# Performance work log

Hardware: AMD Instinct MI355X
Metric: run time of the kernel (lower is better)

The kernel has to match this reference:

```python
import jax, jax.numpy as jnp
import numpy as np

IMG_W, IMG_H = 640, 480
OS = 8            # roialign output_size
SCALE = 1.0       # spatial_scale (boxes already mapped to feature coords)
ALIGNED = True
ALPHA = 1.0       # student-t alpha


def _roi_align_one(feat, boxes):
    # feat: [C, H, W]; boxes: [sn, 4] (x1, y1, x2, y2) in feature coords.
    # torchvision RoIAlign, sampling_ratio=1 (one sample at each bin center).
    C, H, W = feat.shape
    off = 0.5 if ALIGNED else 0.0
    x1 = boxes[:, 0] * SCALE - off
    y1 = boxes[:, 1] * SCALE - off
    x2 = boxes[:, 2] * SCALE - off
    y2 = boxes[:, 3] * SCALE - off
    bw = (x2 - x1) / OS   # bin width  [sn]
    bh = (y2 - y1) / OS   # bin height [sn]
    grid = jnp.arange(OS, dtype=feat.dtype) + 0.5
    xs = x1[:, None] + grid * bw[:, None]   # [sn, OS]
    ys = y1[:, None] + grid * bh[:, None]   # [sn, OS]
    X = jnp.broadcast_to(xs[:, None, :], (xs.shape[0], OS, OS))  # [sn,OS,OS]
    Y = jnp.broadcast_to(ys[:, :, None], (ys.shape[0], OS, OS))
    valid = (Y >= -1.0) & (Y <= H) & (X >= -1.0) & (X <= W)
    y = jnp.clip(Y, 0.0, H - 1)
    x = jnp.clip(X, 0.0, W - 1)
    y0f = jnp.floor(y); x0f = jnp.floor(x)
    y0 = y0f.astype(jnp.int32); x0 = x0f.astype(jnp.int32)
    y1i = jnp.minimum(y0 + 1, H - 1); x1i = jnp.minimum(x0 + 1, W - 1)
    ly = y - y0f; lx = x - x0f
    hy = 1.0 - ly; hx = 1.0 - lx
    def g(yi, xi):
        return feat[:, yi, xi]  # [C, sn, OS, OS]
    val = (hy * hx)[None] * g(y0, x0) + (hy * lx)[None] * g(y0, x1i) \
        + (ly * hx)[None] * g(y1i, x0) + (ly * lx)[None] * g(y1i, x1i)
    val = jnp.where(valid[None], val, 0.0)
    return jnp.transpose(val, (1, 0, 2, 3))  # [sn, C, OS, OS]


def setup_inputs() -> dict:
    key = jax.random.key(0)
    ks = jax.random.split(key, 10)
    B, SN, C, T, FY, FX = 16, 64, 480, 2, 60, 80
    NDF1, NDF2, K = 1024, 256, 64
    z = jax.random.normal(ks[0], (B, C, T, FY, FX), jnp.float32)
    # boxes in image pixel coords
    cx = jax.random.uniform(ks[1], (B, SN), minval=0.1, maxval=0.9) * IMG_W
    cy = jax.random.uniform(ks[2], (B, SN), minval=0.1, maxval=0.9) * IMG_H
    bw = jax.random.uniform(ks[3], (B, SN), minval=0.05, maxval=0.3) * IMG_W
    bh = jax.random.uniform(ks[4], (B, SN), minval=0.05, maxval=0.3) * IMG_H
    x1 = jnp.clip(cx - bw / 2, 0.0, IMG_W); x2 = jnp.clip(cx + bw / 2, 0.0, IMG_W)
    y1 = jnp.clip(cy - bh / 2, 0.0, IMG_H); y2 = jnp.clip(cy + bh / 2, 0.0, IMG_H)
    bboxs = jnp.stack([x1, y1, x2, y2], axis=-1).astype(jnp.float32)
    din = C * OS * OS
    w1 = jax.random.normal(ks[5], (NDF1, din), jnp.float32) * (din ** -0.5)
    b1 = jnp.zeros((NDF1,), jnp.float32)
    w2 = jax.random.normal(ks[6], (NDF2, NDF1), jnp.float32) * (NDF1 ** -0.5)
    b2 = jnp.zeros((NDF2,), jnp.float32)
    centroids = jax.random.normal(ks[7], (K, NDF2), jnp.float32)
    return {"z": z, "bboxs": bboxs, "w1": w1, "b1": b1, "w2": w2, "b2": b2,
            "centroids": centroids}


def reference(z, bboxs, w1, b1, w2, b2, centroids):
    B, C, T, fy, fx = z.shape
    sn = bboxs.shape[1]
    # scale image-space boxes to feature coords (per (x,y) pair as in torch code)
    sc = jnp.array([fx / IMG_W, fy / IMG_H], jnp.float32)
    bb = (bboxs.reshape(B, sn, 2, 2) * sc).reshape(B, sn, 4)
    bb = jnp.nan_to_num(bb)
    feat = z[:, :, -1]  # [B, C, fy, fx]
    pooled = jax.vmap(_roi_align_one)(feat, bb)  # [B, sn, C, OS, OS]
    flat = pooled.reshape(B * sn, -1)
    e = flat @ w1.T + b1
    e = e @ w2.T + b2
    zz = e.reshape(B, sn, -1)  # [B, sn, ndf2]
    # student-t soft assignment (faithful: L2 norm, not squared)
    z2 = jnp.sum(zz * zz, axis=-1, keepdims=True)          # [B,sn,1]
    c2 = jnp.sum(centroids * centroids, axis=-1)           # [K]
    zc = jnp.einsum('bsd,kd->bsk', zz, centroids)          # [B,sn,K]
    nrm = jnp.sqrt(jnp.maximum(z2 + c2 - 2.0 * zc, 0.0))
    s = ((1.0 + nrm) / ALPHA) ** (-(ALPHA + 1.0) / 2.0)
    s = s / jnp.sum(s, axis=-1, keepdims=True)
    c = jnp.argmax(s, axis=2)
    return zz, s, c
```

## Files before the change

kernel.cpp:

```cpp
#include <hip/hip_runtime.h>
#include <hip/hip_bf16.h>

static constexpr int B_  = 16;
static constexpr int SN_ = 64;
static constexpr int C_  = 480;
static constexpr int T_  = 2;
static constexpr int FY_ = 60;
static constexpr int FX_ = 80;
static constexpr int OS_ = 8;
static constexpr int DIN = 30720;
static constexpr int M_  = 1024;
static constexpr int N1_ = 1024;
static constexpr int N2_ = 256;
static constexpr int K_  = 64;
static constexpr int SPLITK = 32;
static constexpr int CH_ZZ  = 3 * DIN / SPLITK;
static constexpr int NIT_ZZ = CH_ZZ / 64;
static constexpr int NIT_FW = 3 * N1_ / 64;
static constexpr int CPB = 2;
static constexpr int IMG = FY_ * FX_;
static constexpr int NB_ROI = 16 * (C_ / CPB);
static constexpr int NB_W1T = (DIN / 64) * (N1_ / 64);
static constexpr int NB_W2P = N2_;

typedef __bf16 bf16x8 __attribute__((ext_vector_type(8)));
typedef float  f32x4  __attribute__((ext_vector_type(4)));
typedef unsigned int u32_as1 __attribute__((address_space(1)));
typedef unsigned int u32_as3 __attribute__((address_space(3)));

__device__ __forceinline__ float bf2f(unsigned short u) {
    union { unsigned int i; float f; } v; v.i = ((unsigned int)u) << 16; return v.f;
}
__device__ __forceinline__ unsigned short f2bf(float f) {
    unsigned int u = __float_as_uint(f);
    u = u + 0x7FFFu + ((u >> 16) & 1u);
    return (unsigned short)(u >> 16);
}
__device__ __forceinline__ void gll16(const void* g, void* l) {
    __builtin_amdgcn_global_load_lds((const u32_as1*)g, (u32_as3*)l, 16, 0, 0);
}

template<int NIT, int SEG>
__device__ __forceinline__ void gemm_core(
    const unsigned short* __restrict__ Abase, long long Astride,
    const unsigned short* __restrict__ Bbase, long long Bstride,
    int kv0, f32x4 (&acc)[4][4],
    unsigned short* As, unsigned short* Bs)
{
    const int t = threadIdx.x;
    const int w = t >> 6, lane = t & 63;
    const int rl8 = lane >> 3, slot = lane & 7;
    const int wm = w >> 1, wn = w & 1;
    const int fr = lane & 15, fg = lane >> 4;
    const int swz8 = (slot ^ rl8) * 8;

    long long arow[4], brow[4];
    int ci[4];
#pragma unroll
    for (int c = 0; c < 4; ++c) {
        ci[c] = w * 4 + c;
        const int row = ci[c] * 8 + rl8;
        arow[c] = (long long)row * Astride;
        brow[c] = (long long)row * Bstride;
    }

    auto stage = [&](int it, int par) {
        const int kv  = kv0 + it * 64;
        const int seg = (kv >= 2 * SEG) ? 2 : ((kv >= SEG) ? 1 : 0);
        const int kin = kv - seg * SEG;
        const int aoff = kin + ((seg == 2) ? SEG : 0) + swz8;
        const int boff = kin + ((seg == 1) ? SEG : 0) + swz8;
#pragma unroll
        for (int c = 0; c < 4; ++c) {
            gll16(Abase + arow[c] + aoff, (char*)As + par * 16384 + ci[c] * 1024);
            gll16(Bbase + brow[c] + boff, (char*)Bs + par * 16384 + ci[c] * 1024);
        }
    };

    stage(0, 0);
    stage(1, 1);

    for (int it = 0; it < NIT; ++it) {
        const int par = it & 1;
        if (it + 1 < NIT) asm volatile("s_waitcnt vmcnt(8)" ::: "memory");
        else              asm volatile("s_waitcnt vmcnt(0)" ::: "memory");
        __builtin_amdgcn_s_barrier();

        const char* Ab = (const char*)As + par * 16384;
        const char* Bb = (const char*)Bs + par * 16384;
        bf16x8 a[2][4], b[2][4];
#pragma unroll
        for (int ks = 0; ks < 2; ++ks)
#pragma unroll
            for (int mf = 0; mf < 4; ++mf) {
                const int row = wm * 64 + mf * 16 + fr;
                a[ks][mf] = *reinterpret_cast<const bf16x8*>(
                    Ab + row * 128 + 16 * ((ks * 4 + fg) ^ (fr & 7)));
            }
#pragma unroll
        for (int ks = 0; ks < 2; ++ks)
#pragma unroll
            for (int nf = 0; nf < 4; ++nf) {
                const int row = wn * 64 + nf * 16 + fr;
                b[ks][nf] = *reinterpret_cast<const bf16x8*>(
                    Bb + row * 128 + 16 * ((ks * 4 + fg) ^ (fr & 7)));
            }
        asm volatile("s_waitcnt lgkmcnt(0)" ::: "memory");
        __builtin_amdgcn_sched_barrier(0);
        __builtin_amdgcn_s_barrier();
        __builtin_amdgcn_sched_barrier(0);
        if (it + 2 < NIT) stage(it + 2, par);

        __builtin_amdgcn_s_setprio(1);
#pragma unroll
        for (int ks = 0; ks < 2; ++ks)
#pragma unroll
            for (int mf = 0; mf < 4; ++mf)
#pragma unroll
                for (int nf = 0; nf < 4; ++nf)
                    acc[mf][nf] = __builtin_amdgcn_mfma_f32_16x16x32_bf16(
                        a[ks][mf], b[ks][nf], acc[ks ? mf : mf][nf], 0, 0, 0);
        __builtin_amdgcn_s_setprio(0);
    }
}

__global__ __launch_bounds__(256) void prep_kernel(
    const float* __restrict__ z, const float* __restrict__ bboxs,
    const float* __restrict__ w1, const float* __restrict__ w2,
    const float* __restrict__ b1, const float* __restrict__ b2,
    unsigned short* __restrict__ flat2, unsigned short* __restrict__ w1T2,
    unsigned short* __restrict__ w2cat, float* __restrict__ bf) {
    __shared__ __align__(16) char smem[39424];
    const int blk = blockIdx.x;
    const int t = threadIdx.x;

    if (blk < NB_ROI) {
        float* img = (float*)smem;
        float (*bxc)[4] = (float (*)[4])(smem + 38400);
        const int b  = blk / (C_ / CPB);
        const int cg = blk % (C_ / CPB);
        const float* zb = z + ((size_t)b * C_ + (size_t)cg * CPB) * (size_t)(T_ * IMG)
                            + (size_t)(T_ - 1) * IMG;
#pragma unroll
        for (int c = 0; c < CPB; ++c) {
            const float4* src = (const float4*)(zb + (size_t)c * (T_ * IMG));
            float4* dst = (float4*)(img + c * IMG);
            for (int i = t; i < IMG / 4; i += 256) dst[i] = src[i];
        }
        if (t < 64) {
            const float* bp = bboxs + ((size_t)b * 64 + t) * 4;
            const float v0 = bp[0], v1 = bp[1], v2 = bp[2], v3 = bp[3];
            bxc[t][0] = isnan(v0) ? 0.f : v0;
            bxc[t][1] = isnan(v1) ? 0.f : v1;
            bxc[t][2] = isnan(v2) ? 0.f : v2;
            bxc[t][3] = isnan(v3) ? 0.f : v3;
        }
        __syncthreads();

        const int p = t & 63, mh = t >> 6;
        const int gy = p >> 3, gx = p & 7;
        for (int mq = 0; mq < 16; ++mq) {
            const int m = mq * 4 + mh;
            const float x1 = bxc[m][0] * 0.125f - 0.5f;
            const float y1 = bxc[m][1] * 0.125f - 0.5f;
            const float x2 = bxc[m][2] * 0.125f - 0.5f;
            const float y2 = bxc[m][3] * 0.125f - 0.5f;
            const float bw = (x2 - x1) * (1.0f / OS_);
            const float bh = (y2 - y1) * (1.0f / OS_);
            const float X = x1 + ((float)gx + 0.5f) * bw;
            const float Y = y1 + ((float)gy + 0.5f) * bh;
            const bool valid = (Y >= -1.0f) && (Y <= (float)FY_) &&
                               (X >= -1.0f) && (X <= (float)FX_);
            const float yc = fminf(fmaxf(Y, 0.f), (float)(FY_ - 1));
            const float xc = fminf(fmaxf(X, 0.f), (float)(FX_ - 1));
            const float y0f = floorf(yc), x0f = floorf(xc);
            const int y0 = (int)y0f, x0 = (int)x0f;
            const int y1i = min(y0 + 1, FY_ - 1);
            const int x1i = min(x0 + 1, FX_ - 1);
            const float ly = yc - y0f, lx = xc - x0f;
            const float hy = 1.f - ly,  hx = 1.f - lx;
            float w00 = hy * hx, w01 = hy * lx, w10 = ly * hx, w11 = ly * lx;
            if (!valid) { w00 = 0.f; w01 = 0.f; w10 = 0.f; w11 = 0.f; }
            const int i00 = y0 * FX_ + x0, i01 = y0 * FX_ + x1i;
            const int i10 = y1i * FX_ + x0, i11 = y1i * FX_ + x1i;
            unsigned short* fo = flat2 + (size_t)(b * 64 + m) * (2 * DIN)
                                       + cg * (CPB * 64) + p;
#pragma unroll
            for (int c = 0; c < CPB; ++c) {
                const float* f = img + c * IMG;
                const float v = w00 * f[i00] + w01 * f[i01] + w10 * f[i10] + w11 * f[i11];
                const unsigned short hi = f2bf(v);
                const unsigned short lo = f2bf(v - bf2f(hi));
                fo[c * 64]       = hi;
                fo[DIN + c * 64] = lo;
            }
        }
    } else if (blk < NB_ROI + NB_W1T) {
        float (*L)[65] = (float (*)[65])smem;
        const int idx = blk - NB_ROI;
        const int q0 = (idx % (DIN / 64)) * 64, j0 = (idx / (DIN / 64)) * 64;
        const int tr = t >> 4, tc4 = (t & 15) * 4;
#pragma unroll
        for (int jj = 0; jj < 4; ++jj) {
            const int j = jj * 16 + tr;
            const float4 v = *(const float4*)(w1 + (size_t)(j0 + j) * DIN + q0 + tc4);
            L[j][tc4] = v.x; L[j][tc4 + 1] = v.y; L[j][tc4 + 2] = v.z; L[j][tc4 + 3] = v.w;
        }
        __syncthreads();
#pragma unroll
        for (int pass = 0; pass < 4; ++pass) {
            const int ql = pass * 16 + tr;
            const int jc = tc4;
            ushort4 h4, l4;
            float v0 = L[jc + 0][ql], v1 = L[jc + 1][ql], v2 = L[jc + 2][ql], v3 = L[jc + 3][ql];
            h4.x = f2bf(v0); l4.x = f2bf(v0 - bf2f(h4.x));
            h4.y = f2bf(v1); l4.y = f2bf(v1 - bf2f(h4.y));
            h4.z = f2bf(v2); l4.z = f2bf(v2 - bf2f(h4.z));
            h4.w = f2bf(v3); l4.w = f2bf(v3 - bf2f(h4.w));
            *(ushort4*)(w1T2 + (size_t)(q0 + ql) * 2048 + j0 + jc)        = h4;
            *(ushort4*)(w1T2 + (size_t)(q0 + ql) * 2048 + 1024 + j0 + jc) = l4;
        }
    } else {
        float* red = (float*)smem;
        const int p = blk - (NB_ROI + NB_W1T);
        float acc = 0.f;
#pragma unroll
        for (int j = t; j < N1_; j += 256) {
            const float v = w2[(size_t)p * N1_ + j];
            const unsigned short hi = f2bf(v);
            const unsigned short lo = f2bf(v - bf2f(hi));
            w2cat[(size_t)p * 2048 + j]        = hi;
            w2cat[(size_t)p * 2048 + 1024 + j] = lo;
            acc = fmaf(v, b1[j], acc);
        }
        red[t] = acc; __syncthreads();
        for (int s = 128; s > 0; s >>= 1) { if (t < s) red[t] += red[t + s]; __syncthreads(); }
        if (t == 0) bf[p] = red[0] + b2[p];
    }
}

__global__ __launch_bounds__(256, 2) void fusew_mfma(const unsigned short* __restrict__ w2cat,
                                                     const unsigned short* __restrict__ w1T2,
                                                     unsigned short* __restrict__ W2) {
    __shared__ __align__(16) unsigned short As[2 * 128 * 64];
    __shared__ __align__(16) unsigned short Bs[2 * 128 * 64];
    const int pb = blockIdx.x, qb = blockIdx.y;
    f32x4 acc[4][4];
#pragma unroll
    for (int i = 0; i < 4; ++i)
#pragma unroll
        for (int j = 0; j < 4; ++j) acc[i][j] = (f32x4){0.f, 0.f, 0.f, 0.f};

    gemm_core<NIT_FW, N1_>(w2cat + (long long)pb * 128 * 2048, 2048,
                           w1T2 + (long long)qb * 128 * 2048, 2048,
                           0, acc, As, Bs);

    const int t = threadIdx.x;
    const int w = t >> 6, lane = t & 63;
    const int wm = w >> 1, wn = w & 1;
    const int fr = lane & 15, fg = lane >> 4;
#pragma unroll
    for (int mf = 0; mf < 4; ++mf)
#pragma unroll
        for (int nf = 0; nf < 4; ++nf)
#pragma unroll
            for (int r = 0; r < 4; ++r) {
                const int p = pb * 128 + wm * 64 + mf * 16 + fg * 4 + r;
                const int q = qb * 128 + wn * 64 + nf * 16 + fr;
                const float v = acc[mf][nf][r];
                const unsigned short hi = f2bf(v);
                const unsigned short lo = f2bf(v - bf2f(hi));
                W2[(size_t)p * (2 * DIN) + q]       = hi;
                W2[(size_t)p * (2 * DIN) + DIN + q] = lo;
            }
}

__global__ __launch_bounds__(256, 2) void zz_mfma(const unsigned short* __restrict__ flat2,
                                                  const unsigned short* __restrict__ W2,
                                                  float* __restrict__ part) {
    __shared__ __align__(16) unsigned short As[2 * 128 * 64];
    __shared__ __align__(16) unsigned short Bs[2 * 128 * 64];
    const int nb = blockIdx.x, mb = blockIdx.y, sp = blockIdx.z;
    f32x4 acc[4][4];
#pragma unroll
    for (int i = 0; i < 4; ++i)
#pragma unroll
        for (int j = 0; j < 4; ++j) acc[i][j] = (f32x4){0.f, 0.f, 0.f, 0.f};

    gemm_core<NIT_ZZ, DIN>(flat2 + (long long)mb * 128 * (2 * DIN), 2 * DIN,
                           W2 + (long long)nb * 128 * (2 * DIN), 2 * DIN,
                           sp * CH_ZZ, acc, As, Bs);

    float* po = part + (size_t)sp * (M_ * N2_);
    const int t = threadIdx.x;
    const int w = t >> 6, lane = t & 63;
    const int wm = w >> 1, wn = w & 1;
    const int fr = lane & 15, fg = lane >> 4;
#pragma unroll
    for (int mf = 0; mf < 4; ++mf)
#pragma unroll
        for (int nf = 0; nf < 4; ++nf)
#pragma unroll
            for (int r = 0; r < 4; ++r) {
                const int m = mb * 128 + wm * 64 + mf * 16 + fg * 4 + r;
                const int n = nb * 128 + wn * 64 + nf * 16 + fr;
                po[(size_t)m * N2_ + n] = acc[mf][nf][r];
            }
}

__global__ __launch_bounds__(256) void reduce_cluster_kernel(
    const float* __restrict__ part, const float* __restrict__ bf,
    const float* __restrict__ cent,
    float* __restrict__ out_zz, float* __restrict__ out_s, float* __restrict__ out_c) {
    __shared__ float row[N2_];
    const int m = blockIdx.x, t = threadIdx.x;
    float a = bf[t];
#pragma unroll
    for (int s = 0; s < SPLITK; ++s) a += part[(size_t)s * (M_ * N2_) + (size_t)m * N2_ + t];
    out_zz[(size_t)m * N2_ + t] = a;
    row[t] = a;
    __syncthreads();
    if (t < 64) {
        const float* cr = cent + (size_t)t * N2_;
        float dot = 0.f, c2 = 0.f, z2 = 0.f;
        for (int d = 0; d < N2_; ++d) {
            const float zv = row[d], cv = cr[d];
            dot = fmaf(zv, cv, dot);
            c2  = fmaf(cv, cv, c2);
            z2  = fmaf(zv, zv, z2);
        }
        const float nrm = sqrtf(fmaxf(z2 + c2 - 2.f * dot, 0.f));
        const float su = 1.0f / (1.0f + nrm);
        float ssum = su;
#pragma unroll
        for (int mk = 1; mk < 64; mk <<= 1) ssum += __shfl_xor(ssum, mk, 64);
        const float s = su / ssum;
        out_s[(size_t)m * 64 + t] = s;
        float bv = s; int bi = t;
#pragma unroll
        for (int mk = 1; mk < 64; mk <<= 1) {
            const float ov = __shfl_xor(bv, mk, 64);
            const int   oi = __shfl_xor(bi, mk, 64);
            if (ov > bv || (ov == bv && oi < bi)) { bv = ov; bi = oi; }
        }
        if (t == 0) out_c[m] = (float)bi;
    }
}

extern "C" void kernel_launch(void* const* d_in, const int* in_sizes, int n_in,
                              void* d_out, int out_size, void* d_ws, size_t ws_size,
                              hipStream_t stream) {
    const float* z     = (const float*)d_in[0];
    const float* bboxs = (const float*)d_in[1];
    const float* w1    = (const float*)d_in[2];
    const float* b1    = (const float*)d_in[3];
    const float* w2    = (const float*)d_in[4];
    const float* b2    = (const float*)d_in[5];
    const float* cent  = (const float*)d_in[6];
    float* out = (float*)d_out;
    float* out_zz = out;
    float* out_s  = out + (size_t)M_ * N2_;
    float* out_c  = out + (size_t)M_ * N2_ + (size_t)M_ * K_;

    char* ws = (char*)d_ws;
    unsigned short* w1T2   = (unsigned short*)(ws);
    unsigned short* flat2  = (unsigned short*)(ws + 125829120u);
    unsigned short* W2     = (unsigned short*)(ws + 251658240u);
    float*          part   = (float*)(ws + 283115520u);
    unsigned short* w2cat  = (unsigned short*)(ws + 316669952u);
    float*          bfused = (float*)(ws + 317718528u);

    prep_kernel<<<dim3(NB_ROI + NB_W1T + NB_W2P), dim3(256), 0, stream>>>(
        z, bboxs, w1, w2, b1, b2, flat2, w1T2, w2cat, bfused);
    fusew_mfma<<<dim3(2, 240), dim3(256), 0, stream>>>(w2cat, w1T2, W2);
    zz_mfma<<<dim3(2, 8, SPLITK), dim3(256), 0, stream>>>(flat2, W2, part);
    reduce_cluster_kernel<<<dim3(1024), dim3(256), 0, stream>>>(part, bfused, cent,
                                                                out_zz, out_s, out_c);
}
```

Before: 273.8 us.

## Restructure split-bf16 GEMMs to stage hi/lo halves together with 8-wave blocks

The shared GEMM core now loads the hi and lo halves of A and B for the same k-chunk into LDS together, instead of walking three concatenated k-segments. Each step issues the three hi*hi, hi*lo and lo*hi MFMAs, so the A/B fragments are reused across the three products. Blocks grow to 512 threads arranged as 2x4 waves with a 64 KB-per-stage LDS double buffer. Block indices are remapped to a 1D grid so that tiles sharing an operand land on the same XCD. The aim is better operand reuse and L2 locality, at the cost of occupancy, which drops to one block per CU with larger LDS use.

```diff
diff --git a/kernel.cpp b/kernel.cpp
--- a/kernel.cpp
+++ b/kernel.cpp
@@ -14,9 +14,8 @@
 static constexpr int N2_ = 256;
 static constexpr int K_  = 64;
 static constexpr int SPLITK = 32;
-static constexpr int CH_ZZ  = 3 * DIN / SPLITK;
-static constexpr int NIT_ZZ = CH_ZZ / 64;
-static constexpr int NIT_FW = 3 * N1_ / 64;
+static constexpr int NCH_ZZ = (DIN / 64) / SPLITK;
+static constexpr int NCH_FW = N1_ / 64;
 static constexpr int CPB = 2;
 static constexpr int IMG = FY_ * FX_;
 static constexpr int NB_ROI = 16 * (C_ / CPB);
@@ -40,76 +39,78 @@
     __builtin_amdgcn_global_load_lds((const u32_as1*)g, (u32_as3*)l, 16, 0, 0);
 }
 
-template<int NIT, int SEG>
+template<int NCHUNK, int SEG>
 __device__ __forceinline__ void gemm_core(
     const unsigned short* __restrict__ Abase, long long Astride,
     const unsigned short* __restrict__ Bbase, long long Bstride,
-    int kv0, f32x4 (&acc)[4][4],
-    unsigned short* As, unsigned short* Bs)
+    int k0, f32x4 (&acc)[4][2], unsigned short* L)
 {
     const int t = threadIdx.x;
     const int w = t >> 6, lane = t & 63;
     const int rl8 = lane >> 3, slot = lane & 7;
-    const int wm = w >> 1, wn = w & 1;
+    const int wm = w >> 2, wn = w & 3;
     const int fr = lane & 15, fg = lane >> 4;
     const int swz8 = (slot ^ rl8) * 8;
 
-    long long arow[4], brow[4];
-    int ci[4];
-#pragma unroll
-    for (int c = 0; c < 4; ++c) {
-        ci[c] = w * 4 + c;
+    long long arow[2], brow[2];
+    int ci[2];
+#pragma unroll
+    for (int c = 0; c < 2; ++c) {
+        ci[c] = w * 2 + c;
         const int row = ci[c] * 8 + rl8;
         arow[c] = (long long)row * Astride;
         brow[c] = (long long)row * Bstride;
     }
 
-    auto stage = [&](int it, int par) {
-        const int kv  = kv0 + it * 64;
-        const int seg = (kv >= 2 * SEG) ? 2 : ((kv >= SEG) ? 1 : 0);
-        const int kin = kv - seg * SEG;
-        const int aoff = kin + ((seg == 2) ? SEG : 0) + swz8;
-        const int boff = kin + ((seg == 1) ? SEG : 0) + swz8;
-#pragma unroll
-        for (int c = 0; c < 4; ++c) {
-            gll16(Abase + arow[c] + aoff, (char*)As + par * 16384 + ci[c] * 1024);
-            gll16(Bbase + brow[c] + boff, (char*)Bs + par * 16384 + ci[c] * 1024);
+    auto stage = [&](int chunk, int par) {
+        const int kin = k0 + chunk * 64;
+        char* Lp = (char*)L + par * 65536;
+#pragma unroll
+        for (int c = 0; c < 2; ++c) {
+            gll16(Abase + arow[c] + kin + swz8,       Lp + 0 * 16384 + ci[c] * 1024);
+            gll16(Abase + arow[c] + SEG + kin + swz8, Lp + 1 * 16384 + ci[c] * 1024);
+            gll16(Bbase + brow[c] + kin + swz8,       Lp + 2 * 16384 + ci[c] * 1024);
+            gll16(Bbase + brow[c] + SEG + kin + swz8, Lp + 3 * 16384 + ci[c] * 1024);
         }
     };
 
     stage(0, 0);
     stage(1, 1);
 
-    for (int it = 0; it < NIT; ++it) {
+    for (int it = 0; it < NCHUNK; ++it) {
         const int par = it & 1;
-        if (it + 1 < NIT) asm volatile("s_waitcnt vmcnt(8)" ::: "memory");
-        else              asm volatile("s_waitcnt vmcnt(0)" ::: "memory");
+        if (it + 1 < NCHUNK) asm volatile("s_waitcnt vmcnt(8)" ::: "memory");
+        else                 asm volatile("s_waitcnt vmcnt(0)" ::: "memory");
         __builtin_amdgcn_s_barrier();
 
-        const char* Ab = (const char*)As + par * 16384;
-        const char* Bb = (const char*)Bs + par * 16384;
-        bf16x8 a[2][4], b[2][4];
-#pragma unroll
-        for (int ks = 0; ks < 2; ++ks)
-#pragma unroll
-            for (int mf = 0; mf < 4; ++mf) {
-                const int row = wm * 64 + mf * 16 + fr;
-                a[ks][mf] = *reinterpret_cast<const bf16x8*>(
-                    Ab + row * 128 + 16 * ((ks * 4 + fg) ^ (fr & 7)));
-            }
-#pragma unroll
-        for (int ks = 0; ks < 2; ++ks)
-#pragma unroll
-            for (int nf = 0; nf < 4; ++nf) {
-                const int row = wn * 64 + nf * 16 + fr;
-                b[ks][nf] = *reinterpret_cast<const bf16x8*>(
-                    Bb + row * 128 + 16 * ((ks * 4 + fg) ^ (fr & 7)));
-            }
+        const char* Lp = (const char*)L + par * 65536;
+        bf16x8 a[2][2][4], b[2][2][2];
+#pragma unroll
+        for (int hl = 0; hl < 2; ++hl)
+#pragma unroll
+            for (int ks = 0; ks < 2; ++ks)
+#pragma unroll
+                for (int mf = 0; mf < 4; ++mf) {
+                    const int row = wm * 64 + mf * 16 + fr;
+                    a[hl][ks][mf] = *reinterpret_cast<const bf16x8*>(
+                        Lp + hl * 16384 + row * 128 + 16 * ((ks * 4 + fg) ^ (fr & 7)));
+                }
+#pragma unroll
+        for (int hl = 0; hl < 2; ++hl)
+#pragma unroll
+            for (int ks = 0; ks < 2; ++ks)
+#pragma unroll
+                for (int nf = 0; nf < 2; ++nf) {
+                    const int row = wn * 32 + nf * 16 + fr;
+                    b[hl][ks][nf] = *reinterpret_cast<const bf16x8*>(
+                        Lp + (2 + hl) * 16384 + row * 128 + 16 * ((ks * 4 + fg) ^ (fr & 7)));
+                }
         asm volatile("s_waitcnt lgkmcnt(0)" ::: "memory");
         __builtin_amdgcn_sched_barrier(0);
         __builtin_amdgcn_s_barrier();
         __builtin_amdgcn_sched_barrier(0);
-        if (it + 2 < NIT) stage(it + 2, par);
+        if (it + 2 < NCHUNK) stage(it + 2, par);
+        __builtin_amdgcn_sched_barrier(0);
 
         __builtin_amdgcn_s_setprio(1);
 #pragma unroll
@@ -117,9 +118,14 @@
 #pragma unroll
             for (int mf = 0; mf < 4; ++mf)
 #pragma unroll
-                for (int nf = 0; nf < 4; ++nf)
+                for (int nf = 0; nf < 2; ++nf) {
                     acc[mf][nf] = __builtin_amdgcn_mfma_f32_16x16x32_bf16(
-                        a[ks][mf], b[ks][nf], acc[ks ? mf : mf][nf], 0, 0, 0);
+                        a[0][ks][mf], b[0][ks][nf], acc[mf][nf], 0, 0, 0);
+                    acc[mf][nf] = __builtin_amdgcn_mfma_f32_16x16x32_bf16(
+                        a[0][ks][mf], b[1][ks][nf], acc[mf][nf], 0, 0, 0);
+                    acc[mf][nf] = __builtin_amdgcn_mfma_f32_16x16x32_bf16(
+                        a[1][ks][mf], b[0][ks][nf], acc[mf][nf], 0, 0, 0);
+                }
         __builtin_amdgcn_s_setprio(0);
     }
 }
@@ -239,34 +245,36 @@
     }
 }
 
-__global__ __launch_bounds__(256, 2) void fusew_mfma(const unsigned short* __restrict__ w2cat,
+__global__ __launch_bounds__(512, 1) void fusew_mfma(const unsigned short* __restrict__ w2cat,
                                                      const unsigned short* __restrict__ w1T2,
                                                      unsigned short* __restrict__ W2) {
-    __shared__ __align__(16) unsigned short As[2 * 128 * 64];
-    __shared__ __align__(16) unsigned short Bs[2 * 128 * 64];
-    const int pb = blockIdx.x, qb = blockIdx.y;
-    f32x4 acc[4][4];
+    __shared__ __align__(16) unsigned short L[2 * 4 * 128 * 64];
+    const int bid = blockIdx.x;
+    const int xcd = bid & 7, j = bid >> 3;
+    const int pb = j & 1;
+    const int qb = xcd * 30 + (j >> 1);
+    f32x4 acc[4][2];
 #pragma unroll
     for (int i = 0; i < 4; ++i)
 #pragma unroll
-        for (int j = 0; j < 4; ++j) acc[i][j] = (f32x4){0.f, 0.f, 0.f, 0.f};
-
-    gemm_core<NIT_FW, N1_>(w2cat + (long long)pb * 128 * 2048, 2048,
+        for (int k = 0; k < 2; ++k) acc[i][k] = (f32x4){0.f, 0.f, 0.f, 0.f};
+
+    gemm_core<NCH_FW, N1_>(w2cat + (long long)pb * 128 * 2048, 2048,
                            w1T2 + (long long)qb * 128 * 2048, 2048,
-                           0, acc, As, Bs);
+                           0, acc, L);
 
     const int t = threadIdx.x;
     const int w = t >> 6, lane = t & 63;
-    const int wm = w >> 1, wn = w & 1;
+    const int wm = w >> 2, wn = w & 3;
     const int fr = lane & 15, fg = lane >> 4;
 #pragma unroll
     for (int mf = 0; mf < 4; ++mf)
 #pragma unroll
-        for (int nf = 0; nf < 4; ++nf)
+        for (int nf = 0; nf < 2; ++nf)
 #pragma unroll
             for (int r = 0; r < 4; ++r) {
                 const int p = pb * 128 + wm * 64 + mf * 16 + fg * 4 + r;
-                const int q = qb * 128 + wn * 64 + nf * 16 + fr;
+                const int q = qb * 128 + wn * 32 + nf * 16 + fr;
                 const float v = acc[mf][nf][r];
                 const unsigned short hi = f2bf(v);
                 const unsigned short lo = f2bf(v - bf2f(hi));
@@ -275,35 +283,38 @@
             }
 }
 
-__global__ __launch_bounds__(256, 2) void zz_mfma(const unsigned short* __restrict__ flat2,
+__global__ __launch_bounds__(512, 1) void zz_mfma(const unsigned short* __restrict__ flat2,
                                                   const unsigned short* __restrict__ W2,
                                                   float* __restrict__ part) {
-    __shared__ __align__(16) unsigned short As[2 * 128 * 64];
-    __shared__ __align__(16) unsigned short Bs[2 * 128 * 64];
-    const int nb = blockIdx.x, mb = blockIdx.y, sp = blockIdx.z;
-    f32x4 acc[4][4];
+    __shared__ __align__(16) unsigned short L[2 * 4 * 128 * 64];
+    const int bid = blockIdx.x;
+    const int xcd = bid & 7, j = bid >> 3;
+    const int mb = j & 7;
+    const int pair = xcd * 8 + (j >> 3);
+    const int nb = pair & 1, sp = pair >> 1;
+    f32x4 acc[4][2];
 #pragma unroll
     for (int i = 0; i < 4; ++i)
 #pragma unroll
-        for (int j = 0; j < 4; ++j) acc[i][j] = (f32x4){0.f, 0.f, 0.f, 0.f};
-
-    gemm_core<NIT_ZZ, DIN>(flat2 + (long long)mb * 128 * (2 * DIN), 2 * DIN,
+        for (int k = 0; k < 2; ++k) acc[i][k] = (f32x4){0.f, 0.f, 0.f, 0.f};
+
+    gemm_core<NCH_ZZ, DIN>(flat2 + (long long)mb * 128 * (2 * DIN), 2 * DIN,
                            W2 + (long long)nb * 128 * (2 * DIN), 2 * DIN,
-                           sp * CH_ZZ, acc, As, Bs);
+                           sp * (NCH_ZZ * 64), acc, L);
 
     float* po = part + (size_t)sp * (M_ * N2_);
     const int t = threadIdx.x;
     const int w = t >> 6, lane = t & 63;
-    const int wm = w >> 1, wn = w & 1;
+    const int wm = w >> 2, wn = w & 3;
     const int fr = lane & 15, fg = lane >> 4;
 #pragma unroll
     for (int mf = 0; mf < 4; ++mf)
 #pragma unroll
-        for (int nf = 0; nf < 4; ++nf)
+        for (int nf = 0; nf < 2; ++nf)
 #pragma unroll
             for (int r = 0; r < 4; ++r) {
                 const int m = mb * 128 + wm * 64 + mf * 16 + fg * 4 + r;
-                const int n = nb * 128 + wn * 64 + nf * 16 + fr;
+                const int n = nb * 128 + wn * 32 + nf * 16 + fr;
                 po[(size_t)m * N2_ + n] = acc[mf][nf][r];
             }
 }
@@ -372,8 +383,8 @@
 
     prep_kernel<<<dim3(NB_ROI + NB_W1T + NB_W2P), dim3(256), 0, stream>>>(
         z, bboxs, w1, w2, b1, b2, flat2, w1T2, w2cat, bfused);
-    fusew_mfma<<<dim3(2, 240), dim3(256), 0, stream>>>(w2cat, w1T2, W2);
-    zz_mfma<<<dim3(2, 8, SPLITK), dim3(256), 0, stream>>>(flat2, W2, part);
+    fusew_mfma<<<dim3(480), dim3(512), 0, stream>>>(w2cat, w1T2, W2);
+    zz_mfma<<<dim3(512), dim3(512), 0, stream>>>(flat2, W2, part);
     reduce_cluster_kernel<<<dim3(1024), dim3(256), 0, stream>>>(part, bfused, cent,
                                                                 out_zz, out_s, out_c);
 }
```

New measurement: 235.4 us. -14.0%, faster.
